# Optimization experiments

Measured on AMD Instinct MI355X. Metric: run time of the kernel, lower is better.

## Reference

```python
import jax, jax.numpy as jnp
import numpy as np

MAX_DEPTH = 6
NUM_TREES = 64
LEAF_DIMS = 128
D_IN = 512
BATCH = 4096
N_INTERNAL = 2 ** MAX_DEPTH - 1  # 63
N_LEAVES = 2 ** MAX_DEPTH        # 64


def setup_inputs() -> dict:
    key = jax.random.key(0)
    ks = jax.random.split(key, 4)
    x = jax.random.normal(ks[0], (BATCH, D_IN), dtype=jnp.float32)
    # Stacked internal-node dense layers, node i at index i (level order, node_index ordering)
    W = jax.random.normal(ks[1], (N_INTERNAL, D_IN, NUM_TREES), dtype=jnp.float32) / np.sqrt(D_IN)
    b = jnp.zeros((N_INTERNAL, NUM_TREES), dtype=jnp.float32)
    leaf_weight = jax.random.normal(ks[2], (N_LEAVES, LEAF_DIMS, NUM_TREES), dtype=jnp.float32)
    gates = jax.random.normal(ks[3], (N_LEAVES, LEAF_DIMS, NUM_TREES), dtype=jnp.float32)
    return {"x": x, "W": W, "b": b, "leaf_weight": leaf_weight, "gates": gates}


def reference(x, W, b, leaf_weight, gates):
    # All internal-node gating probabilities in one batched matmul:
    # g[b, n, t] = sigmoid(x[b] @ W[n] + b[n])  for every internal node n, tree t
    g = jax.nn.sigmoid(jnp.einsum('bd,ndt->bnt', x, W) + b[None, :, :])  # [B, 63, T]

    B = x.shape[0]
    T = W.shape[-1]
    # Path probability to each leaf, built level by level.
    # Level l has 2^l nodes at internal indices [2^l - 1, 2^(l+1) - 2];
    # interleaving (left=p*g, right=p*(1-g)) matches node_index child ordering.
    p = jnp.ones((B, 1, T), dtype=x.dtype)
    for level in range(MAX_DEPTH):
        start = 2 ** level - 1
        n_lvl = 2 ** level
        gl = g[:, start:start + n_lvl, :]                  # [B, n_lvl, T]
        children = jnp.stack([p * gl, p * (1.0 - gl)], axis=2)  # [B, n_lvl, 2, T]
        p = children.reshape(B, 2 * n_lvl, T)
    # p: [B, n_leaves, T] leaf path probabilities

    # Softmax mixture-of-experts gate over trees, then weighted leaf mixture:
    # out[b, d] = sum_{l, t} p[b, l, t] * leaf_weight[l, d, t] * softmax(gates, -1)[l, d, t]
    w = leaf_weight * jax.nn.softmax(gates, axis=-1)  # [L, D, T]
    out = jnp.einsum('blt,ldt->bd', p, w)
    return out
```

## Files before the change

kernel.cpp:

```cpp
#include <hip/hip_runtime.h>
#include <stdint.h>

#define BATCH 4096
#define DIN   512
#define NT    64
#define NL    64
#define LD    128

typedef __attribute__((ext_vector_type(8))) short bf16x8;
typedef __attribute__((ext_vector_type(4))) float f32x4;

typedef const __attribute__((address_space(1))) unsigned char* gcp_t;
typedef __attribute__((address_space(3))) unsigned char* lp_t;

__device__ __forceinline__ void gl_lds16(const void* g, void* l) {
  __builtin_amdgcn_global_load_lds((gcp_t)g, (lp_t)l, 16, 0, 0);
}

__device__ __forceinline__ unsigned short f2bf(float f) {
  union { float f; unsigned u; } a; a.f = f;
  unsigned r = a.u + 0x7FFFu + ((a.u >> 16) & 1u);
  return (unsigned short)(r >> 16);
}

__global__ __launch_bounds__(256) void prep_all_k(
    const float* __restrict__ x, const float* __restrict__ W,
    const float* __restrict__ gates, const float* __restrict__ lw,
    unsigned short* __restrict__ xb, unsigned short* __restrict__ Wt,
    unsigned short* __restrict__ Wv2) {
  __shared__ float smem[12288];
  const int bx = blockIdx.x;
  const int tid = threadIdx.x;

  if (bx < 2048) {
    int i = bx * 256 + tid;
    float4 v = ((const float4*)x)[i];
    ushort4 o;
    o.x = f2bf(v.x); o.y = f2bf(v.y); o.z = f2bf(v.z); o.w = f2bf(v.w);
    ((ushort4*)xb)[i] = o;
  } else if (bx < 2304) {
    int bb = bx - 2048;
    int n = bb >> 2, d0 = (bb & 3) * 128;
    float* buf = smem;
    if (n < 63) {
      for (int it = 0; it < 32; ++it) {
        int idx = it * 256 + tid;
        buf[idx] = W[n * 32768 + (d0 + (idx >> 6)) * 64 + (idx & 63)];
      }
    }
    __syncthreads();
    int t = tid >> 2, q = tid & 3;
    unsigned short vals[32];
    #pragma unroll
    for (int j = 0; j < 32; ++j)
      vals[j] = (n < 63) ? f2bf(buf[(q * 32 + j) * 64 + t]) : (unsigned short)0;
    uint4* dst = (uint4*)(Wt + t * 32768 + n * 512 + d0 + q * 32);
    const uint4* src = (const uint4*)vals;
    dst[0] = src[0]; dst[1] = src[1]; dst[2] = src[2]; dst[3] = src[3];
  } else {
    int d = bx - 2304;
    float* gb = smem;
    float* lb = smem + 4096;
    float* wv = smem + 8192;
    for (int it = 0; it < 16; ++it) {
      int idx = it * 256 + tid;
      int l = idx >> 6;
      int ga = l * 8192 + d * 64 + (idx & 63);
      gb[idx] = gates[ga];
      lb[idx] = lw[ga];
    }
    __syncthreads();
    int wave = tid >> 6, lane = tid & 63;
    for (int l = wave; l < 64; l += 4) {
      float v = gb[l * 64 + lane];
      float mx = v;
      for (int m = 32; m >= 1; m >>= 1) mx = fmaxf(mx, __shfl_xor(mx, m));
      float e = __expf(v - mx);
      float s = e;
      for (int m = 32; m >= 1; m >>= 1) s += __shfl_xor(s, m);
      wv[l * 64 + lane] = lb[l * 64 + lane] * e / s;
    }
    __syncthreads();
    #pragma unroll
    for (int c = 0; c < 2; ++c) {
      int k0 = tid * 16 + c * 8;
      union { unsigned short u[8]; uint4 v; } o;
      #pragma unroll
      for (int j = 0; j < 8; ++j) {
        int k = k0 + j;
        o.u[j] = f2bf(wv[(k & 63) * 64 + (k >> 6)]);
      }
      *(uint4*)(Wv2 + (long)d * 4096 + k0) = o.v;
    }
  }
}

__global__ __launch_bounds__(256, 3) void gemm1_tree_k(
    const unsigned short* __restrict__ xb,
    const unsigned short* __restrict__ Wt,
    const float* __restrict__ bias,
    unsigned short* __restrict__ P)
{
  __shared__ unsigned short As[128 * 32];
  __shared__ unsigned short Bs[128 * 32];
  __shared__ _Float16 gbuf[128 * 128];
  __shared__ float bb[128];

  const int tid = threadIdx.x;
  const int wave = tid >> 6, lane = tid & 63;
  const int b0 = blockIdx.x * 128;
  const int t0 = blockIdx.y * 2;

  if (tid < 128) {
    int n = tid & 63, t = t0 + (tid >> 6);
    bb[tid] = (n < 63) ? bias[n * 64 + t] : 0.0f;
  }

  const f32x4 zero = {0.f, 0.f, 0.f, 0.f};
  f32x4 acc[4][4];
  #pragma unroll
  for (int i = 0; i < 4; ++i)
    #pragma unroll
    for (int j = 0; j < 4; ++j) acc[i][j] = zero;

  const int g0 = wave * 64 + lane;
  const int g1 = g0 + 256;
  const unsigned short* Ag0 = xb + (long)(b0 + (g0 >> 2)) * 512 + (g0 & 3) * 8;
  const unsigned short* Ag1 = xb + (long)(b0 + (g1 >> 2)) * 512 + (g1 & 3) * 8;
  const unsigned short* Bg0 = Wt + (long)(t0 * 64 + (g0 >> 2)) * 512 + (g0 & 3) * 8;
  const unsigned short* Bg1 = Wt + (long)(t0 * 64 + (g1 >> 2)) * 512 + (g1 & 3) * 8;
  unsigned short* lA0 = As + (wave * 64) * 8;
  unsigned short* lA1 = As + (wave * 64 + 256) * 8;
  unsigned short* lB0 = Bs + (wave * 64) * 8;
  unsigned short* lB1 = Bs + (wave * 64 + 256) * 8;

  const int wm = (wave >> 1) * 64, wn = (wave & 1) * 64;
  const int mrow = lane & 15, kg = lane >> 4;

  for (int kk = 0; kk < 512; kk += 32) {
    __syncthreads();
    gl_lds16(Ag0 + kk, lA0);
    gl_lds16(Ag1 + kk, lA1);
    gl_lds16(Bg0 + kk, lB0);
    gl_lds16(Bg1 + kk, lB1);
    asm volatile("s_waitcnt vmcnt(0)" ::: "memory");
    __syncthreads();

    bf16x8 fa[4], fb[4];
    #pragma unroll
    for (int i = 0; i < 4; ++i)
      fa[i] = *(const bf16x8*)(As + (wm + i * 16 + mrow) * 32 + kg * 8);
    #pragma unroll
    for (int j = 0; j < 4; ++j)
      fb[j] = *(const bf16x8*)(Bs + (wn + j * 16 + mrow) * 32 + kg * 8);
    #pragma unroll
    for (int i = 0; i < 4; ++i)
      #pragma unroll
      for (int j = 0; j < 4; ++j)
        acc[i][j] = __builtin_amdgcn_mfma_f32_16x16x32_bf16(fa[i], fb[j], acc[i][j], 0, 0, 0);
  }

  #pragma unroll
  for (int i = 0; i < 4; ++i)
    #pragma unroll
    for (int j = 0; j < 4; ++j) {
      int col = wn + j * 16 + mrow;
      float bv = bb[col];
      #pragma unroll
      for (int r = 0; r < 4; ++r) {
        int row = wm + i * 16 + kg * 4 + r;
        float z = acc[i][j][r] + bv;
        gbuf[row * 128 + col] = (_Float16)(1.0f / (1.0f + __expf(-z)));
      }
    }
  __syncthreads();

  #pragma unroll
  for (int cc = 0; cc < 8; ++cc) {
    int chunk = cc * 256 + tid;
    int row = chunk >> 4;
    int tr  = (chunk >> 3) & 1;
    int oct = chunk & 7;
    const _Float16* grow = gbuf + row * 128 + tr * 64;
    int l0 = oct * 8;
    float pre = 1.0f;
    #pragma unroll
    for (int lev = 0; lev < 3; ++lev) {
      int node = (1 << lev) - 1 + (l0 >> (6 - lev));
      float g = (float)grow[node];
      pre *= ((l0 >> (5 - lev)) & 1) ? (1.0f - g) : g;
    }
    union { unsigned short u[8]; uint4 v; } ou;
    #pragma unroll
    for (int j = 0; j < 8; ++j) {
      int l = l0 + j;
      float p = pre;
      #pragma unroll
      for (int lev = 3; lev < 6; ++lev) {
        int node = (1 << lev) - 1 + (l >> (6 - lev));
        float g = (float)grow[node];
        p *= ((l >> (5 - lev)) & 1) ? (1.0f - g) : g;
      }
      ou.u[j] = f2bf(p);
    }
    *(uint4*)(P + (long)(b0 + row) * 4096 + (t0 + tr) * 64 + l0) = ou.v;
  }
}

__global__ __launch_bounds__(256, 2) void gemm2_k(
    const unsigned short* __restrict__ P,
    const unsigned short* __restrict__ Wv2,
    float* __restrict__ out)
{
  __shared__ unsigned short As[128 * 32];
  __shared__ unsigned short Bs[128 * 32];
  const int tid = threadIdx.x;
  const int wave = tid >> 6, lane = tid & 63;
  const int b0 = blockIdx.x * 128;
  const int kc = blockIdx.y;

  const f32x4 zero = {0.f, 0.f, 0.f, 0.f};
  f32x4 acc[4][4];
  #pragma unroll
  for (int i = 0; i < 4; ++i)
    #pragma unroll
    for (int j = 0; j < 4; ++j) acc[i][j] = zero;

  const int g0 = wave * 64 + lane;
  const int g1 = g0 + 256;
  const unsigned short* Ag0 = P + (long)(b0 + (g0 >> 2)) * 4096 + kc * 512 + (g0 & 3) * 8;
  const unsigned short* Ag1 = P + (long)(b0 + (g1 >> 2)) * 4096 + kc * 512 + (g1 & 3) * 8;
  const unsigned short* Bg0 = Wv2 + (long)(g0 >> 2) * 4096 + kc * 512 + (g0 & 3) * 8;
  const unsigned short* Bg1 = Wv2 + (long)(g1 >> 2) * 4096 + kc * 512 + (g1 & 3) * 8;
  unsigned short* lA0 = As + (wave * 64) * 8;
  unsigned short* lA1 = As + (wave * 64 + 256) * 8;
  unsigned short* lB0 = Bs + (wave * 64) * 8;
  unsigned short* lB1 = Bs + (wave * 64 + 256) * 8;

  const int wm = (wave >> 1) * 64, wn = (wave & 1) * 64;
  const int mrow = lane & 15, kg = lane >> 4;

  for (int kk = 0; kk < 512; kk += 32) {
    __syncthreads();
    gl_lds16(Ag0 + kk, lA0);
    gl_lds16(Ag1 + kk, lA1);
    gl_lds16(Bg0 + kk, lB0);
    gl_lds16(Bg1 + kk, lB1);
    asm volatile("s_waitcnt vmcnt(0)" ::: "memory");
    __syncthreads();

    bf16x8 fa[4], fb[4];
    #pragma unroll
    for (int i = 0; i < 4; ++i)
      fa[i] = *(const bf16x8*)(As + (wm + i * 16 + mrow) * 32 + kg * 8);
    #pragma unroll
    for (int j = 0; j < 4; ++j)
      fb[j] = *(const bf16x8*)(Bs + (wn + j * 16 + mrow) * 32 + kg * 8);
    #pragma unroll
    for (int i = 0; i < 4; ++i)
      #pragma unroll
      for (int j = 0; j < 4; ++j)
        acc[i][j] = __builtin_amdgcn_mfma_f32_16x16x32_bf16(fa[i], fb[j], acc[i][j], 0, 0, 0);
  }

  #pragma unroll
  for (int i = 0; i < 4; ++i)
    #pragma unroll
    for (int j = 0; j < 4; ++j) {
      int col = wn + j * 16 + mrow;
      #pragma unroll
      for (int r = 0; r < 4; ++r) {
        int row = wm + i * 16 + kg * 4 + r;
        atomicAdd(&out[(long)(b0 + row) * 128 + col], acc[i][j][r]);
      }
    }
}

extern "C" void kernel_launch(void* const* d_in, const int* in_sizes, int n_in,
                              void* d_out, int out_size, void* d_ws, size_t ws_size,
                              hipStream_t stream) {
  const float* x     = (const float*)d_in[0];
  const float* W     = (const float*)d_in[1];
  const float* b     = (const float*)d_in[2];
  const float* lw    = (const float*)d_in[3];
  const float* gates = (const float*)d_in[4];
  float* out = (float*)d_out;

  char* ws = (char*)d_ws;
  unsigned short* xb  = (unsigned short*)(ws);
  unsigned short* Wt  = (unsigned short*)(ws + (4l  << 20));
  unsigned short* Wv2 = (unsigned short*)(ws + (8l  << 20));
  unsigned short* P   = (unsigned short*)(ws + (16l << 20));

  hipMemsetAsync(out, 0, (size_t)4096 * 128 * sizeof(float), stream);
  hipLaunchKernelGGL(prep_all_k,   dim3(2432),   dim3(256), 0, stream,
                     x, W, gates, lw, xb, Wt, Wv2);
  hipLaunchKernelGGL(gemm1_tree_k, dim3(32, 32), dim3(256), 0, stream, xb, Wt, b, P);
  hipLaunchKernelGGL(gemm2_k,      dim3(32, 8),  dim3(256), 0, stream, P, Wv2, out);
}
```

Baseline: 148.5 us.

## Restructure tree path product per thread and halve gemm2 M-tile

Each thread now loads a whole 63-node gate row for one (batch row, tree) pair into registers using vector LDS reads, from a padded gbuf, and builds the 64 leaf probabilities by sharing prefix products. The old code re-read gates per leaf with scalar LDS loads. Separately, gemm2 uses a 64-row M tile with a doubled grid and higher occupancy, giving more blocks for the 256-CU device. The trade-offs are higher register pressure in gemm1 from the 63-float array, more reloads of the B tile, and more atomics in gemm2.

```diff
diff --git a/kernel.cpp b/kernel.cpp
--- a/kernel.cpp
+++ b/kernel.cpp
@@ -8,6 +8,7 @@
 #define LD    128
 
 typedef __attribute__((ext_vector_type(8))) short bf16x8;
+typedef __attribute__((ext_vector_type(8))) _Float16 f16x8;
 typedef __attribute__((ext_vector_type(4))) float f32x4;
 
 typedef const __attribute__((address_space(1))) unsigned char* gcp_t;
@@ -103,7 +104,7 @@
 {
   __shared__ unsigned short As[128 * 32];
   __shared__ unsigned short Bs[128 * 32];
-  __shared__ _Float16 gbuf[128 * 128];
+  __shared__ __align__(16) _Float16 gbuf[128 * 136];
   __shared__ float bb[128];
 
   const int tid = threadIdx.x;
@@ -170,101 +171,110 @@
       for (int r = 0; r < 4; ++r) {
         int row = wm + i * 16 + kg * 4 + r;
         float z = acc[i][j][r] + bv;
-        gbuf[row * 128 + col] = (_Float16)(1.0f / (1.0f + __expf(-z)));
+        gbuf[row * 136 + col] = (_Float16)(1.0f / (1.0f + __expf(-z)));
       }
     }
   __syncthreads();
 
-  #pragma unroll
-  for (int cc = 0; cc < 8; ++cc) {
-    int chunk = cc * 256 + tid;
-    int row = chunk >> 4;
-    int tr  = (chunk >> 3) & 1;
-    int oct = chunk & 7;
-    const _Float16* grow = gbuf + row * 128 + tr * 64;
-    int l0 = oct * 8;
-    float pre = 1.0f;
-    #pragma unroll
-    for (int lev = 0; lev < 3; ++lev) {
-      int node = (1 << lev) - 1 + (l0 >> (6 - lev));
-      float g = (float)grow[node];
-      pre *= ((l0 >> (5 - lev)) & 1) ? (1.0f - g) : g;
-    }
-    union { unsigned short u[8]; uint4 v; } ou;
-    #pragma unroll
-    for (int j = 0; j < 8; ++j) {
-      int l = l0 + j;
-      float p = pre;
-      #pragma unroll
-      for (int lev = 3; lev < 6; ++lev) {
-        int node = (1 << lev) - 1 + (l >> (6 - lev));
-        float g = (float)grow[node];
-        p *= ((l >> (5 - lev)) & 1) ? (1.0f - g) : g;
-      }
-      ou.u[j] = f2bf(p);
-    }
-    *(uint4*)(P + (long)(b0 + row) * 4096 + (t0 + tr) * 64 + l0) = ou.v;
-  }
-}
-
-__global__ __launch_bounds__(256, 2) void gemm2_k(
+  {
+    const int row = tid >> 1, tr = tid & 1;
+    const _Float16* grow = gbuf + row * 136 + tr * 64;
+    float g[63];
+    #pragma unroll
+    for (int c = 0; c < 8; ++c) {
+      f16x8 gv = *(const f16x8*)(grow + c * 8);
+      #pragma unroll
+      for (int j = 0; j < 8; ++j) {
+        int n = c * 8 + j;
+        if (n < 63) g[n] = (float)gv[j];
+      }
+    }
+    float P3[8];
+    {
+      float a0 = g[0],            a1 = 1.0f - g[0];
+      float c0 = a0 * g[1],       c1 = a0 * (1.0f - g[1]);
+      float c2 = a1 * g[2],       c3 = a1 * (1.0f - g[2]);
+      P3[0] = c0 * g[3];  P3[1] = c0 * (1.0f - g[3]);
+      P3[2] = c1 * g[4];  P3[3] = c1 * (1.0f - g[4]);
+      P3[4] = c2 * g[5];  P3[5] = c2 * (1.0f - g[5]);
+      P3[6] = c3 * g[6];  P3[7] = c3 * (1.0f - g[6]);
+    }
+    unsigned short* prow = P + (long)(b0 + row) * 4096 + (t0 + tr) * 64;
+    #pragma unroll
+    for (int o = 0; o < 8; ++o) {
+      float g3 = g[7 + o];
+      float q0 = P3[o] * g3, q1 = P3[o] * (1.0f - g3);
+      float g4a = g[15 + 2 * o], g4b = g[16 + 2 * o];
+      float r0 = q0 * g4a, r1 = q0 * (1.0f - g4a);
+      float r2 = q1 * g4b, r3 = q1 * (1.0f - g4b);
+      union { unsigned short u[8]; uint4 v; } ou;
+      #pragma unroll
+      for (int h = 0; h < 4; ++h) {
+        float g5 = g[31 + 4 * o + h];
+        float rr = (h == 0) ? r0 : (h == 1) ? r1 : (h == 2) ? r2 : r3;
+        ou.u[2 * h]     = f2bf(rr * g5);
+        ou.u[2 * h + 1] = f2bf(rr * (1.0f - g5));
+      }
+      *(uint4*)(prow + o * 8) = ou.v;
+    }
+  }
+}
+
+__global__ __launch_bounds__(256, 4) void gemm2_k(
     const unsigned short* __restrict__ P,
     const unsigned short* __restrict__ Wv2,
     float* __restrict__ out)
 {
-  __shared__ unsigned short As[128 * 32];
+  __shared__ unsigned short As[64 * 32];
   __shared__ unsigned short Bs[128 * 32];
   const int tid = threadIdx.x;
   const int wave = tid >> 6, lane = tid & 63;
-  const int b0 = blockIdx.x * 128;
+  const int b0 = blockIdx.x * 64;
   const int kc = blockIdx.y;
 
   const f32x4 zero = {0.f, 0.f, 0.f, 0.f};
-  f32x4 acc[4][4];
+  f32x4 acc[2][4];
   #pragma unroll
-  for (int i = 0; i < 4; ++i)
+  for (int i = 0; i < 2; ++i)
     #pragma unroll
     for (int j = 0; j < 4; ++j) acc[i][j] = zero;
 
   const int g0 = wave * 64 + lane;
   const int g1 = g0 + 256;
   const unsigned short* Ag0 = P + (long)(b0 + (g0 >> 2)) * 4096 + kc * 512 + (g0 & 3) * 8;
-  const unsigned short* Ag1 = P + (long)(b0 + (g1 >> 2)) * 4096 + kc * 512 + (g1 & 3) * 8;
   const unsigned short* Bg0 = Wv2 + (long)(g0 >> 2) * 4096 + kc * 512 + (g0 & 3) * 8;
   const unsigned short* Bg1 = Wv2 + (long)(g1 >> 2) * 4096 + kc * 512 + (g1 & 3) * 8;
   unsigned short* lA0 = As + (wave * 64) * 8;
-  unsigned short* lA1 = As + (wave * 64 + 256) * 8;
   unsigned short* lB0 = Bs + (wave * 64) * 8;
   unsigned short* lB1 = Bs + (wave * 64 + 256) * 8;
 
-  const int wm = (wave >> 1) * 64, wn = (wave & 1) * 64;
+  const int wm = (wave >> 1) * 32, wn = (wave & 1) * 64;
   const int mrow = lane & 15, kg = lane >> 4;
 
   for (int kk = 0; kk < 512; kk += 32) {
     __syncthreads();
     gl_lds16(Ag0 + kk, lA0);
-    gl_lds16(Ag1 + kk, lA1);
     gl_lds16(Bg0 + kk, lB0);
     gl_lds16(Bg1 + kk, lB1);
     asm volatile("s_waitcnt vmcnt(0)" ::: "memory");
     __syncthreads();
 
-    bf16x8 fa[4], fb[4];
-    #pragma unroll
-    for (int i = 0; i < 4; ++i)
+    bf16x8 fa[2], fb[4];
+    #pragma unroll
+    for (int i = 0; i < 2; ++i)
       fa[i] = *(const bf16x8*)(As + (wm + i * 16 + mrow) * 32 + kg * 8);
     #pragma unroll
     for (int j = 0; j < 4; ++j)
       fb[j] = *(const bf16x8*)(Bs + (wn + j * 16 + mrow) * 32 + kg * 8);
     #pragma unroll
-    for (int i = 0; i < 4; ++i)
+    for (int i = 0; i < 2; ++i)
       #pragma unroll
       for (int j = 0; j < 4; ++j)
         acc[i][j] = __builtin_amdgcn_mfma_f32_16x16x32_bf16(fa[i], fb[j], acc[i][j], 0, 0, 0);
   }
 
   #pragma unroll
-  for (int i = 0; i < 4; ++i)
+  for (int i = 0; i < 2; ++i)
     #pragma unroll
     for (int j = 0; j < 4; ++j) {
       int col = wn + j * 16 + mrow;
@@ -296,5 +306,5 @@
   hipLaunchKernelGGL(prep_all_k,   dim3(2432),   dim3(256), 0, stream,
                      x, W, gates, lw, xb, Wt, Wv2);
   hipLaunchKernelGGL(gemm1_tree_k, dim3(32, 32), dim3(256), 0, stream, xb, Wt, b, P);
-  hipLaunchKernelGGL(gemm2_k,      dim3(32, 8),  dim3(256), 0, stream, P, Wv2, out);
-}
+  hipLaunchKernelGGL(gemm2_k,      dim3(64, 8),  dim3(256), 0, stream, P, Wv2, out);
+}
```

Result: no change. 147.8 us (-0.4%).
